# Performance work log

Measured on AMD Instinct MI355X. Metric: run time of the kernel, lower is better.

Reference implementation:

```python
import jax, jax.numpy as jnp
import numpy as np

NUM_INPUTS = 1024
NUM_HIDDEN = 1024
FORGET_GATE_BIAS = -1.0
EPS = 1e-5


def layer_norm_1d(x, weight, bias):
    # Matches torch LayerNorm1D: std is unbiased (ddof=1), divide by (std + eps)
    mean = jnp.mean(x, axis=1, keepdims=True)
    std = jnp.std(x, axis=1, keepdims=True, ddof=1)
    return (x - mean) / (std + EPS) * weight + bias


def setup_inputs() -> dict:
    key = jax.random.key(0)
    ks = jax.random.split(key, 8)
    B, I, H = 4096, NUM_INPUTS, NUM_HIDDEN
    lim_i = 1.0 / np.sqrt(I)
    lim_h = 1.0 / np.sqrt(H)
    return {
        "inputs": jax.random.normal(ks[0], (B, I), jnp.float32),
        "hx": jax.random.normal(ks[1], (B, H), jnp.float32),
        "cx": jax.random.normal(ks[2], (B, H), jnp.float32),
        "w_i2h": jax.random.uniform(ks[3], (4 * H, I), jnp.float32, -lim_i, lim_i),
        "b_i2h": jax.random.uniform(ks[4], (4 * H,), jnp.float32, -lim_i, lim_i),
        "w_h2h": jax.random.uniform(ks[5], (4 * H, H), jnp.float32, -lim_h, lim_h),
        "b_h2h": jax.random.uniform(ks[6], (4 * H,), jnp.float32, -lim_h, lim_h),
        "ln_i2h_w": jnp.ones((1, 4 * H), jnp.float32),
        "ln_i2h_b": jnp.zeros((1, 4 * H), jnp.float32),
        "ln_h2h_w": jnp.ones((1, 4 * H), jnp.float32),
        "ln_h2h_b": jnp.zeros((1, 4 * H), jnp.float32),
        "ln_h2o_w": jnp.ones((1, H), jnp.float32),
        "ln_h2o_b": jnp.zeros((1, H), jnp.float32),
    }


def reference(inputs, hx, cx, w_i2h, b_i2h, w_h2h, b_h2h,
              ln_i2h_w, ln_i2h_b, ln_h2h_w, ln_h2h_b, ln_h2o_w, ln_h2o_b):
    H = NUM_HIDDEN
    i2h = inputs @ w_i2h.T + b_i2h          # [B, 4H]
    h2h = hx @ w_h2h.T + b_h2h              # [B, 4H]
    x = layer_norm_1d(i2h, ln_i2h_w, ln_i2h_b) + layer_norm_1d(h2h, ln_h2h_w, ln_h2h_b)
    g_i, g_f, g_o, g_c = jnp.split(x, 4, axis=1)
    in_gate = jax.nn.sigmoid(g_i)
    forget_gate = jax.nn.sigmoid(g_f + FORGET_GATE_BIAS)
    out_gate = jax.nn.sigmoid(g_o)
    in_transform = jnp.tanh(g_c)
    cx_new = forget_gate * cx + in_gate * in_transform
    hx_new = out_gate * jnp.tanh(layer_norm_1d(cx_new, ln_h2o_w, ln_h2o_b))
    return hx_new, cx_new
```

## Files before the change

kernel.cpp:

```cpp
#include <hip/hip_runtime.h>
#include <hip/hip_bf16.h>
#include <math.h>

#define NI 1024
#define NH 1024
#define H4 4096
#define FGB (-1.0f)
#define LN_EPS 1e-5f
#define NKT 32

typedef unsigned short u16;
typedef __attribute__((ext_vector_type(8))) short short8;
typedef __attribute__((ext_vector_type(8))) unsigned short ushort8v;
typedef __attribute__((ext_vector_type(16))) float f32x16;

__device__ __forceinline__ float bf2f(u16 u) {
    union { unsigned int i; float f; } v; v.i = ((unsigned int)u) << 16; return v.f;
}
__device__ __forceinline__ u16 f2bf(float f) {
    __hip_bfloat16 h = __float2bfloat16(f);
    return __builtin_bit_cast(u16, h);
}
__device__ __forceinline__ ushort8v cvt8(float4 lo, float4 hi) {
    ushort8v r;
    r[0] = f2bf(lo.x); r[1] = f2bf(lo.y); r[2] = f2bf(lo.z); r[3] = f2bf(lo.w);
    r[4] = f2bf(hi.x); r[5] = f2bf(hi.y); r[6] = f2bf(hi.z); r[7] = f2bf(hi.w);
    return r;
}
__device__ __forceinline__ float fast_sigmoid(float x) {
    return 1.0f / (1.0f + __expf(-x));
}
__device__ __forceinline__ float fast_tanh(float x) {
    return 1.0f - 2.0f / (__expf(2.0f * x) + 1.0f);
}

__global__ __launch_bounds__(256) void shuffle_cast(
    const float* __restrict__ a, const float* __restrict__ b,
    const float* __restrict__ c, const float* __restrict__ d,
    u16* __restrict__ oa, u16* __restrict__ ob,
    u16* __restrict__ oc, u16* __restrict__ od)
{
    const int my = blockIdx.y;
    const float* src = (my == 0) ? a : (my == 1) ? b : (my == 2) ? c : d;
    u16*         dst = (my == 0) ? oa : (my == 1) ? ob : (my == 2) ? oc : od;

    const int lane = threadIdx.x & 63;
    const int wave = threadIdx.x >> 6;
    const int p    = blockIdx.x * 4 + wave;
    const int mtile = p >> 5;
    const int kt    = p & 31;

    const int row  = mtile * 32 + (lane & 31);
    const int colf = kt * 32 + (lane >> 5) * 8;
    const float* s = src + (size_t)row * 1024 + colf;
    u16* o = dst + (size_t)p * 1024 + lane * 8;

    float4 l0 = *(const float4*)(s);
    float4 h0 = *(const float4*)(s + 4);
    float4 l1 = *(const float4*)(s + 16);
    float4 h1 = *(const float4*)(s + 20);
    *(ushort8v*)(o)       = cvt8(l0, h0);
    *(ushort8v*)(o + 512) = cvt8(l1, h1);
}

__global__ __launch_bounds__(256) void gemm_frag(
    const u16* __restrict__ Af0, const u16* __restrict__ Wf0,
    const float* __restrict__ bias0, u16* __restrict__ C0,
    const u16* __restrict__ Af1, const u16* __restrict__ Wf1,
    const float* __restrict__ bias1, u16* __restrict__ C1,
    int N)
{
    const u16*   Af   = blockIdx.z ? Af1 : Af0;
    const u16*   Wf   = blockIdx.z ? Wf1 : Wf0;
    const float* bias = blockIdx.z ? bias1 : bias0;
    u16*         C    = blockIdx.z ? C1 : C0;

    const int lane = threadIdx.x & 63;
    const int wave = threadIdx.x >> 6;
    const int wm   = wave & 1;
    const int wn   = wave >> 1;
    const int m0   = blockIdx.y * 128;
    const int n0   = blockIdx.x * 128;

    const int mt0 = blockIdx.y * 4 + wm * 2;
    const int nt0 = blockIdx.x * 4 + wn * 2;
    const u16* pa0 = Af + (size_t)mt0 * 32768 + lane * 8;
    const u16* pa1 = pa0 + 32768;
    const u16* pb0 = Wf + (size_t)nt0 * 32768 + lane * 8;
    const u16* pb1 = pb0 + 32768;

    f32x16 acc[2][2];
#pragma unroll
    for (int i = 0; i < 2; ++i)
#pragma unroll
        for (int j = 0; j < 2; ++j)
#pragma unroll
            for (int r = 0; r < 16; ++r)
                acc[i][j][r] = 0.f;

    ushort8v f[3][8];

#define LDTILE(buf, kt)                                              \
    do {                                                             \
        const size_t o_ = (size_t)(kt) * 1024;                       \
        f[buf][0] = *(const ushort8v*)(pa0 + o_);                    \
        f[buf][1] = *(const ushort8v*)(pa0 + o_ + 512);              \
        f[buf][2] = *(const ushort8v*)(pa1 + o_);                    \
        f[buf][3] = *(const ushort8v*)(pa1 + o_ + 512);              \
        f[buf][4] = *(const ushort8v*)(pb0 + o_);                    \
        f[buf][5] = *(const ushort8v*)(pb0 + o_ + 512);              \
        f[buf][6] = *(const ushort8v*)(pb1 + o_);                    \
        f[buf][7] = *(const ushort8v*)(pb1 + o_ + 512);              \
    } while (0)

#define MFMA8(buf)                                                                              \
    do {                                                                                        \
        acc[0][0] = __builtin_amdgcn_mfma_f32_32x32x16_bf16(                                    \
            (short8)f[buf][0], (short8)f[buf][4], acc[0][0], 0, 0, 0);                          \
        acc[0][1] = __builtin_amdgcn_mfma_f32_32x32x16_bf16(                                    \
            (short8)f[buf][0], (short8)f[buf][6], acc[0][1], 0, 0, 0);                          \
        acc[1][0] = __builtin_amdgcn_mfma_f32_32x32x16_bf16(                                    \
            (short8)f[buf][2], (short8)f[buf][4], acc[1][0], 0, 0, 0);                          \
        acc[1][1] = __builtin_amdgcn_mfma_f32_32x32x16_bf16(                                    \
            (short8)f[buf][2], (short8)f[buf][6], acc[1][1], 0, 0, 0);                          \
        acc[0][0] = __builtin_amdgcn_mfma_f32_32x32x16_bf16(                                    \
            (short8)f[buf][1], (short8)f[buf][5], acc[0][0], 0, 0, 0);                          \
        acc[0][1] = __builtin_amdgcn_mfma_f32_32x32x16_bf16(                                    \
            (short8)f[buf][1], (short8)f[buf][7], acc[0][1], 0, 0, 0);                          \
        acc[1][0] = __builtin_amdgcn_mfma_f32_32x32x16_bf16(                                    \
            (short8)f[buf][3], (short8)f[buf][5], acc[1][0], 0, 0, 0);                          \
        acc[1][1] = __builtin_amdgcn_mfma_f32_32x32x16_bf16(                                    \
            (short8)f[buf][3], (short8)f[buf][7], acc[1][1], 0, 0, 0);                          \
    } while (0)

    LDTILE(0, 0);
    LDTILE(1, 1);
#pragma unroll
    for (int kt = 0; kt < NKT; ++kt) {
        const int cur = kt % 3;
        const int nxt = (kt + 2) % 3;
        if (kt + 2 < NKT) LDTILE(nxt, kt + 2);
        MFMA8(cur);
    }
#undef LDTILE
#undef MFMA8

    const int l31 = lane & 31;
    float bv[2];
#pragma unroll
    for (int tn = 0; tn < 2; ++tn)
        bv[tn] = bias[n0 + wn * 64 + tn * 32 + l31];

    const int rbase = (lane >> 5) * 4;
#pragma unroll
    for (int tm = 0; tm < 2; ++tm)
#pragma unroll
        for (int reg = 0; reg < 16; ++reg) {
            const int row = m0 + wm * 64 + tm * 32 + (reg & 3) + 8 * (reg >> 2) + rbase;
#pragma unroll
            for (int tn = 0; tn < 2; ++tn) {
                const int col = n0 + wn * 64 + tn * 32 + l31;
                C[(size_t)row * N + col] = f2bf(acc[tm][tn][reg] + bv[tn]);
            }
        }
}

__global__ __launch_bounds__(256) void lstm_pointwise(
    const u16* __restrict__ i2h, const u16* __restrict__ h2h,
    const float* __restrict__ cx,
    const float* __restrict__ lwx, const float* __restrict__ lbx,
    const float* __restrict__ lwy, const float* __restrict__ lby,
    const float* __restrict__ lwc, const float* __restrict__ lbc,
    float* __restrict__ hx_out, float* __restrict__ cx_out)
{
    __shared__ u16 sX[H4];
    __shared__ u16 sY[H4];
    __shared__ float red[16];

    const int row  = blockIdx.x;
    const int tid  = threadIdx.x;
    const int lane = tid & 63;
    const int wid  = tid >> 6;

    const u16* xr = i2h + (size_t)row * H4;
    const u16* yr = h2h + (size_t)row * H4;

    float sx = 0.f, sxx = 0.f, sy = 0.f, syy = 0.f;
#pragma unroll
    for (int s = 0; s < 2; ++s) {
        const int off = s * 2048 + tid * 8;
        ushort8v xv = *(const ushort8v*)(xr + off);
        ushort8v yv = *(const ushort8v*)(yr + off);
        *(ushort8v*)(sX + off) = xv;
        *(ushort8v*)(sY + off) = yv;
#pragma unroll
        for (int e = 0; e < 8; ++e) {
            float x = bf2f(xv[e]), y = bf2f(yv[e]);
            sx += x; sxx += x * x; sy += y; syy += y * y;
        }
    }
#pragma unroll
    for (int m = 32; m; m >>= 1) {
        sx  += __shfl_xor(sx,  m, 64);
        sxx += __shfl_xor(sxx, m, 64);
        sy  += __shfl_xor(sy,  m, 64);
        syy += __shfl_xor(syy, m, 64);
    }
    if (lane == 0) {
        red[wid] = sx; red[4 + wid] = sxx; red[8 + wid] = sy; red[12 + wid] = syy;
    }
    __syncthreads();
    const float tsx  = red[0] + red[1] + red[2] + red[3];
    const float tsxx = red[4] + red[5] + red[6] + red[7];
    const float tsy  = red[8] + red[9] + red[10] + red[11];
    const float tsyy = red[12] + red[13] + red[14] + red[15];
    __syncthreads();

    const float n1  = (float)H4;
    const float mx  = tsx / n1;
    const float ivx = 1.0f / (sqrtf(fmaxf((tsxx - tsx * tsx / n1) / (n1 - 1.f), 0.f)) + LN_EPS);
    const float my  = tsy / n1;
    const float ivy = 1.0f / (sqrtf(fmaxf((tsyy - tsy * tsy / n1) / (n1 - 1.f), 0.f)) + LN_EPS);

    const int j0 = tid * 4;
    float gate[4][4];
#pragma unroll
    for (int g = 0; g < 4; ++g) {
        ushort4 xv = *(const ushort4*)(sX + g * NH + j0);
        ushort4 yv = *(const ushort4*)(sY + g * NH + j0);
        float4 wxv = *(const float4*)(lwx + g * NH + j0);
        float4 bxv = *(const float4*)(lbx + g * NH + j0);
        float4 wyv = *(const float4*)(lwy + g * NH + j0);
        float4 byv = *(const float4*)(lby + g * NH + j0);
        gate[g][0] = (bf2f(xv.x) - mx) * ivx * wxv.x + bxv.x + (bf2f(yv.x) - my) * ivy * wyv.x + byv.x;
        gate[g][1] = (bf2f(xv.y) - mx) * ivx * wxv.y + bxv.y + (bf2f(yv.y) - my) * ivy * wyv.y + byv.y;
        gate[g][2] = (bf2f(xv.z) - mx) * ivx * wxv.z + bxv.z + (bf2f(yv.z) - my) * ivy * wyv.z + byv.z;
        gate[g][3] = (bf2f(xv.w) - mx) * ivx * wxv.w + bxv.w + (bf2f(yv.w) - my) * ivy * wyv.w + byv.w;
    }

    float4 cxv = *(const float4*)(cx + (size_t)row * NH + j0);
    const float cin[4] = {cxv.x, cxv.y, cxv.z, cxv.w};
    float cvl[4], og[4];
    float sc = 0.f, scc = 0.f;
#pragma unroll
    for (int e = 0; e < 4; ++e) {
        float ing = fast_sigmoid(gate[0][e]);
        float fg  = fast_sigmoid(gate[1][e] + FGB);
        og[e]     = fast_sigmoid(gate[2][e]);
        float tr  = fast_tanh(gate[3][e]);
        float c   = fg * cin[e] + ing * tr;
        cvl[e] = c; sc += c; scc += c * c;
    }
    *(float4*)(cx_out + (size_t)row * NH + j0) = make_float4(cvl[0], cvl[1], cvl[2], cvl[3]);

#pragma unroll
    for (int m = 32; m; m >>= 1) {
        sc  += __shfl_xor(sc,  m, 64);
        scc += __shfl_xor(scc, m, 64);
    }
    if (lane == 0) { red[wid] = sc; red[4 + wid] = scc; }
    __syncthreads();
    const float tsc  = red[0] + red[1] + red[2] + red[3];
    const float tscc = red[4] + red[5] + red[6] + red[7];

    const float nc  = (float)NH;
    const float mc  = tsc / nc;
    const float ivc = 1.0f / (sqrtf(fmaxf((tscc - tsc * tsc / nc) / (nc - 1.f), 0.f)) + LN_EPS);

    float4 wcv = *(const float4*)(lwc + j0);
    float4 bcv = *(const float4*)(lbc + j0);
    float h0 = og[0] * fast_tanh((cvl[0] - mc) * ivc * wcv.x + bcv.x);
    float h1 = og[1] * fast_tanh((cvl[1] - mc) * ivc * wcv.y + bcv.y);
    float h2 = og[2] * fast_tanh((cvl[2] - mc) * ivc * wcv.z + bcv.z);
    float h3 = og[3] * fast_tanh((cvl[3] - mc) * ivc * wcv.w + bcv.w);
    *(float4*)(hx_out + (size_t)row * NH + j0) = make_float4(h0, h1, h2, h3);
}

extern "C" void kernel_launch(void* const* d_in, const int* in_sizes, int n_in,
                              void* d_out, int out_size, void* d_ws, size_t ws_size,
                              hipStream_t stream) {
    const float* inputs = (const float*)d_in[0];
    const float* hx     = (const float*)d_in[1];
    const float* cx     = (const float*)d_in[2];
    const float* w_i2h  = (const float*)d_in[3];
    const float* b_i2h  = (const float*)d_in[4];
    const float* w_h2h  = (const float*)d_in[5];
    const float* b_h2h  = (const float*)d_in[6];
    const float* lwx    = (const float*)d_in[7];
    const float* lbx    = (const float*)d_in[8];
    const float* lwy    = (const float*)d_in[9];
    const float* lby    = (const float*)d_in[10];
    const float* lwc    = (const float*)d_in[11];
    const float* lbc    = (const float*)d_in[12];

    const int B = in_sizes[0] / NI;

    u16* a_fr   = (u16*)d_ws;
    u16* hx_fr  = a_fr   + (size_t)B * NI;
    u16* wi_fr  = hx_fr  + (size_t)B * NH;
    u16* wh_fr  = wi_fr  + (size_t)H4 * NI;
    u16* i2h_bf = wh_fr  + (size_t)H4 * NH;
    u16* h2h_bf = i2h_bf + (size_t)B * H4;

    float* hx_out = (float*)d_out;
    float* cx_out = hx_out + (size_t)B * NH;

    shuffle_cast<<<dim3(1024, 4), dim3(256), 0, stream>>>(
        inputs, hx, w_i2h, w_h2h, a_fr, hx_fr, wi_fr, wh_fr);

    gemm_frag<<<dim3(H4 / 128, B / 128, 2), dim3(256), 0, stream>>>(
        a_fr, wi_fr, b_i2h, i2h_bf,
        hx_fr, wh_fr, b_h2h, h2h_bf,
        H4);

    lstm_pointwise<<<dim3(B), dim3(256), 0, stream>>>(
        i2h_bf, h2h_bf, cx, lwx, lbx, lwy, lby, lwc, lbc, hx_out, cx_out);
}
```

Measured before the change: 256.6 us.

## Stage GEMM fragments through LDS with async global-to-LDS loads and 256x256 tiles

Replaces the register-only fragment GEMM, where each wave loaded its own A/B fragments from global memory, with a 512-thread block computing a 256x256 tile. The pre-shuffled fragments are staged into a 4-slot LDS ring using global_load_lds, and barriers plus vmcnt waits pipeline the loads three k-steps ahead. Each loaded fragment is now shared across waves, which cuts global and L2 traffic per MFMA, and setprio raises priority around the MFMA groups. In exchange it adds LDS traffic, many barriers per k-step and higher register pressure from 8 accumulators per wave. The hand-tuned waitcnt counts are fragile.

```diff
diff --git a/kernel.cpp b/kernel.cpp
--- a/kernel.cpp
+++ b/kernel.cpp
@@ -32,6 +32,13 @@
 }
 __device__ __forceinline__ float fast_tanh(float x) {
     return 1.0f - 2.0f / (__expf(2.0f * x) + 1.0f);
+}
+
+__device__ __forceinline__ void gload16(const u16* g, u16* l) {
+    __builtin_amdgcn_global_load_lds(
+        (const __attribute__((address_space(1))) void*)g,
+        (__attribute__((address_space(3))) void*)l,
+        16, 0, 0);
 }
 
 __global__ __launch_bounds__(256) void shuffle_cast(
@@ -63,7 +70,7 @@
     *(ushort8v*)(o + 512) = cvt8(l1, h1);
 }
 
-__global__ __launch_bounds__(256) void gemm_frag(
+__global__ __launch_bounds__(512, 2) void gemm_lds(
     const u16* __restrict__ Af0, const u16* __restrict__ Wf0,
     const float* __restrict__ bias0, u16* __restrict__ C0,
     const u16* __restrict__ Af1, const u16* __restrict__ Wf1,
@@ -75,76 +82,112 @@
     const float* bias = blockIdx.z ? bias1 : bias0;
     u16*         C    = blockIdx.z ? C1 : C0;
 
-    const int lane = threadIdx.x & 63;
-    const int wave = threadIdx.x >> 6;
-    const int wm   = wave & 1;
-    const int wn   = wave >> 1;
-    const int m0   = blockIdx.y * 128;
-    const int n0   = blockIdx.x * 128;
-
-    const int mt0 = blockIdx.y * 4 + wm * 2;
-    const int nt0 = blockIdx.x * 4 + wn * 2;
-    const u16* pa0 = Af + (size_t)mt0 * 32768 + lane * 8;
-    const u16* pa1 = pa0 + 32768;
-    const u16* pb0 = Wf + (size_t)nt0 * 32768 + lane * 8;
-    const u16* pb1 = pb0 + 32768;
-
-    f32x16 acc[2][2];
-#pragma unroll
-    for (int i = 0; i < 2; ++i)
+    __shared__ __align__(16) u16 sA[4][8][2][512];
+    __shared__ __align__(16) u16 sB[4][8][2][512];
+
+    const int tid  = threadIdx.x;
+    const int lane = tid & 63;
+    const int wave = tid >> 6;
+    const int wm   = wave >> 2;
+    const int wn   = wave & 3;
+
+    const u16* gA = Af + (size_t)(blockIdx.y * 8 + wave) * 32768 + lane * 8;
+    const u16* gB = Wf + (size_t)(blockIdx.x * 8 + wave) * 32768 + lane * 8;
+
+    f32x16 acc[4][2];
+#pragma unroll
+    for (int i = 0; i < 4; ++i)
 #pragma unroll
         for (int j = 0; j < 2; ++j)
 #pragma unroll
             for (int r = 0; r < 16; ++r)
                 acc[i][j][r] = 0.f;
 
-    ushort8v f[3][8];
-
-#define LDTILE(buf, kt)                                              \
-    do {                                                             \
-        const size_t o_ = (size_t)(kt) * 1024;                       \
-        f[buf][0] = *(const ushort8v*)(pa0 + o_);                    \
-        f[buf][1] = *(const ushort8v*)(pa0 + o_ + 512);              \
-        f[buf][2] = *(const ushort8v*)(pa1 + o_);                    \
-        f[buf][3] = *(const ushort8v*)(pa1 + o_ + 512);              \
-        f[buf][4] = *(const ushort8v*)(pb0 + o_);                    \
-        f[buf][5] = *(const ushort8v*)(pb0 + o_ + 512);              \
-        f[buf][6] = *(const ushort8v*)(pb1 + o_);                    \
-        f[buf][7] = *(const ushort8v*)(pb1 + o_ + 512);              \
+#define STAGE_A(kt)                                                          \
+    do {                                                                     \
+        gload16(gA + (size_t)(kt) * 1024,       &sA[(kt) & 3][wave][0][0]);  \
+        gload16(gA + (size_t)(kt) * 1024 + 512, &sA[(kt) & 3][wave][1][0]);  \
     } while (0)
-
-#define MFMA8(buf)                                                                              \
-    do {                                                                                        \
-        acc[0][0] = __builtin_amdgcn_mfma_f32_32x32x16_bf16(                                    \
-            (short8)f[buf][0], (short8)f[buf][4], acc[0][0], 0, 0, 0);                          \
-        acc[0][1] = __builtin_amdgcn_mfma_f32_32x32x16_bf16(                                    \
-            (short8)f[buf][0], (short8)f[buf][6], acc[0][1], 0, 0, 0);                          \
-        acc[1][0] = __builtin_amdgcn_mfma_f32_32x32x16_bf16(                                    \
-            (short8)f[buf][2], (short8)f[buf][4], acc[1][0], 0, 0, 0);                          \
-        acc[1][1] = __builtin_amdgcn_mfma_f32_32x32x16_bf16(                                    \
-            (short8)f[buf][2], (short8)f[buf][6], acc[1][1], 0, 0, 0);                          \
-        acc[0][0] = __builtin_amdgcn_mfma_f32_32x32x16_bf16(                                    \
-            (short8)f[buf][1], (short8)f[buf][5], acc[0][0], 0, 0, 0);                          \
-        acc[0][1] = __builtin_amdgcn_mfma_f32_32x32x16_bf16(                                    \
-            (short8)f[buf][1], (short8)f[buf][7], acc[0][1], 0, 0, 0);                          \
-        acc[1][0] = __builtin_amdgcn_mfma_f32_32x32x16_bf16(                                    \
-            (short8)f[buf][3], (short8)f[buf][5], acc[1][0], 0, 0, 0);                          \
-        acc[1][1] = __builtin_amdgcn_mfma_f32_32x32x16_bf16(                                    \
-            (short8)f[buf][3], (short8)f[buf][7], acc[1][1], 0, 0, 0);                          \
+#define STAGE_B(kt)                                                          \
+    do {                                                                     \
+        gload16(gB + (size_t)(kt) * 1024,       &sB[(kt) & 3][wave][0][0]);  \
+        gload16(gB + (size_t)(kt) * 1024 + 512, &sB[(kt) & 3][wave][1][0]);  \
     } while (0)
 
-    LDTILE(0, 0);
-    LDTILE(1, 1);
-#pragma unroll
+#define LDFRAGS(kh)                                                          \
+    do {                                                                     \
+        a0 = *(const ushort8v*)&sA[slot][wm * 4 + 0][kh][lane * 8];          \
+        a1 = *(const ushort8v*)&sA[slot][wm * 4 + 1][kh][lane * 8];          \
+        a2 = *(const ushort8v*)&sA[slot][wm * 4 + 2][kh][lane * 8];          \
+        a3 = *(const ushort8v*)&sA[slot][wn == wn ? wm * 4 + 3 : 0][kh][lane * 8]; \
+    } while (0)
+
+#define MFMA8()                                                                                      \
+    do {                                                                                             \
+        acc[0][0] = __builtin_amdgcn_mfma_f32_32x32x16_bf16((short8)a0, (short8)b0, acc[0][0], 0, 0, 0); \
+        acc[1][0] = __builtin_amdgcn_mfma_f32_32x32x16_bf16((short8)a1, (short8)b0, acc[1][0], 0, 0, 0); \
+        acc[2][0] = __builtin_amdgcn_mfma_f32_32x32x16_bf16((short8)a2, (short8)b0, acc[2][0], 0, 0, 0); \
+        acc[3][0] = __builtin_amdgcn_mfma_f32_32x32x16_bf16((short8)a3, (short8)b0, acc[3][0], 0, 0, 0); \
+        acc[0][1] = __builtin_amdgcn_mfma_f32_32x32x16_bf16((short8)a0, (short8)b1, acc[0][1], 0, 0, 0); \
+        acc[1][1] = __builtin_amdgcn_mfma_f32_32x32x16_bf16((short8)a1, (short8)b1, acc[1][1], 0, 0, 0); \
+        acc[2][1] = __builtin_amdgcn_mfma_f32_32x32x16_bf16((short8)a2, (short8)b1, acc[2][1], 0, 0, 0); \
+        acc[3][1] = __builtin_amdgcn_mfma_f32_32x32x16_bf16((short8)a3, (short8)b1, acc[3][1], 0, 0, 0); \
+    } while (0)
+
+    STAGE_A(0); STAGE_B(0);
+    STAGE_A(1); STAGE_B(1);
+    STAGE_A(2); STAGE_B(2);
+
+    asm volatile("s_waitcnt vmcnt(8)" ::: "memory");
+    __builtin_amdgcn_s_barrier();
+
+    ushort8v a0, a1, a2, a3, b0, b1;
+
     for (int kt = 0; kt < NKT; ++kt) {
-        const int cur = kt % 3;
-        const int nxt = (kt + 2) % 3;
-        if (kt + 2 < NKT) LDTILE(nxt, kt + 2);
-        MFMA8(cur);
-    }
-#undef LDTILE
+        const int slot = kt & 3;
+
+        a0 = *(const ushort8v*)&sA[slot][wm * 4 + 0][0][lane * 8];
+        a1 = *(const ushort8v*)&sA[slot][wm * 4 + 1][0][lane * 8];
+        a2 = *(const ushort8v*)&sA[slot][wm * 4 + 2][0][lane * 8];
+        a3 = *(const ushort8v*)&sA[slot][wm * 4 + 3][0][lane * 8];
+        b0 = *(const ushort8v*)&sB[slot][wn * 2 + 0][0][lane * 8];
+        b1 = *(const ushort8v*)&sB[slot][wn * 2 + 1][0][lane * 8];
+        if (kt + 3 < NKT) STAGE_A(kt + 3);
+        __builtin_amdgcn_s_barrier();
+        asm volatile("s_waitcnt lgkmcnt(0)" ::: "memory");
+        __builtin_amdgcn_s_setprio(1);
+        MFMA8();
+        __builtin_amdgcn_s_setprio(0);
+        __builtin_amdgcn_s_barrier();
+
+        a0 = *(const ushort8v*)&sA[slot][wm * 4 + 0][1][lane * 8];
+        a1 = *(const ushort8v*)&sA[slot][wm * 4 + 1][1][lane * 8];
+        a2 = *(const ushort8v*)&sA[slot][wm * 4 + 2][1][lane * 8];
+        a3 = *(const ushort8v*)&sA[slot][wm * 4 + 3][1][lane * 8];
+        b0 = *(const ushort8v*)&sB[slot][wn * 2 + 0][1][lane * 8];
+        b1 = *(const ushort8v*)&sB[slot][wn * 2 + 1][1][lane * 8];
+        if (kt + 3 < NKT) STAGE_B(kt + 3);
+        __builtin_amdgcn_s_barrier();
+        asm volatile("s_waitcnt lgkmcnt(0)" ::: "memory");
+        __builtin_amdgcn_s_setprio(1);
+        MFMA8();
+        __builtin_amdgcn_s_setprio(0);
+        if (kt < NKT - 3) {
+            asm volatile("s_waitcnt vmcnt(8)" ::: "memory");
+        } else if (kt == NKT - 3) {
+            asm volatile("s_waitcnt vmcnt(4)" ::: "memory");
+        } else if (kt == NKT - 2) {
+            asm volatile("s_waitcnt vmcnt(0)" ::: "memory");
+        }
+        __builtin_amdgcn_s_barrier();
+    }
+#undef STAGE_A
+#undef STAGE_B
+#undef LDFRAGS
 #undef MFMA8
 
+    const int m0  = blockIdx.y * 256;
+    const int n0  = blockIdx.x * 256;
     const int l31 = lane & 31;
     float bv[2];
 #pragma unroll
@@ -153,10 +196,10 @@
 
     const int rbase = (lane >> 5) * 4;
 #pragma unroll
-    for (int tm = 0; tm < 2; ++tm)
+    for (int tm = 0; tm < 4; ++tm)
 #pragma unroll
         for (int reg = 0; reg < 16; ++reg) {
-            const int row = m0 + wm * 64 + tm * 32 + (reg & 3) + 8 * (reg >> 2) + rbase;
+            const int row = m0 + wm * 128 + tm * 32 + (reg & 3) + 8 * (reg >> 2) + rbase;
 #pragma unroll
             for (int tn = 0; tn < 2; ++tn) {
                 const int col = n0 + wn * 64 + tn * 32 + l31;
@@ -308,7 +351,7 @@
     shuffle_cast<<<dim3(1024, 4), dim3(256), 0, stream>>>(
         inputs, hx, w_i2h, w_h2h, a_fr, hx_fr, wi_fr, wh_fr);
 
-    gemm_frag<<<dim3(H4 / 128, B / 128, 2), dim3(256), 0, stream>>>(
+    gemm_lds<<<dim3(H4 / 256, B / 256, 2), dim3(512), 0, stream>>>(
         a_fr, wi_fr, b_i2h, i2h_bf,
         hx_fr, wh_fr, b_h2h, h2h_bf,
         H4);
```

Result: faster. 243.8 us (-5.0%).
